# Kernel tuning notes

Hardware: AMD Instinct MI355X
Metric: run time of the kernel (lower is better)

Reference implementation:

```python
import jax, jax.numpy as jnp
import numpy as np

N = 100000   # nodes
E = 1600000  # edges
G = 2048     # graphs in batch
NF = 64      # node_feature_dim
D = 32       # hidden dim (hard-coded in module)
SF = 512     # solvent_feature_dim
BN_EPS = 1e-5


def setup_inputs() -> dict:
    key = jax.random.key(0)
    ks = jax.random.split(key, 24)
    s = 0.1
    return {
        "x": jax.random.normal(ks[0], (N, NF), jnp.float32),
        "edge_index": jax.random.randint(ks[1], (2, E), 0, N, dtype=jnp.int64),
        "batch": jnp.sort(jax.random.randint(ks[2], (N,), 0, G, dtype=jnp.int64)),
        "solvent_fingerprint": jax.random.uniform(ks[3], (G, SF), jnp.float32),
        # GIN layer 1 first Linear (NF->D); layers 2-5 first Linear stacked (D->D)
        "w1a": jax.random.normal(ks[4], (NF, D), jnp.float32) * s,
        "b1a": jnp.zeros((D,), jnp.float32),
        "ws_a": jax.random.normal(ks[5], (4, D, D), jnp.float32) * s,
        "bs_a": jnp.zeros((4, D), jnp.float32),
        # second Linear of all 5 GIN MLPs
        "ws_b": jax.random.normal(ks[6], (5, D, D), jnp.float32) * s,
        "bs_b": jnp.zeros((5, D), jnp.float32),
        # BatchNorm affine params per layer
        "bn_g": jnp.ones((5, D), jnp.float32),
        "bn_b": jnp.zeros((5, D), jnp.float32),
        # dense head
        "fcg_w": jax.random.normal(ks[7], (D, 128), jnp.float32) * s,
        "fcg_b": jnp.zeros((128,), jnp.float32),
        "fs1_w": jax.random.normal(ks[8], (SF, 256), jnp.float32) * s,
        "fs1_b": jnp.zeros((256,), jnp.float32),
        "fs2_w": jax.random.normal(ks[9], (256, 128), jnp.float32) * s,
        "fs2_b": jnp.zeros((128,), jnp.float32),
        "fc1_w": jax.random.normal(ks[10], (256, 1024), jnp.float32) * s,
        "fc1_b": jnp.zeros((1024,), jnp.float32),
        "fc2_w": jax.random.normal(ks[11], (1024, 256), jnp.float32) * s,
        "fc2_b": jnp.zeros((256,), jnp.float32),
        "out_w": jax.random.normal(ks[12], (256, 1), jnp.float32) * s,
        "out_b": jnp.zeros((1,), jnp.float32),
    }


def _bn_relu(h, g, b):
    # BatchNorm1d training-mode math (biased batch variance), then ReLU
    mu = h.mean(axis=0)
    var = h.var(axis=0)
    return jax.nn.relu((h - mu) * jax.lax.rsqrt(var + BN_EPS) * g + b)


def reference(x, edge_index, batch, solvent_fingerprint,
              w1a, b1a, ws_a, bs_a, ws_b, bs_b, bn_g, bn_b,
              fcg_w, fcg_b, fs1_w, fs1_b, fs2_w, fs2_b,
              fc1_w, fc1_b, fc2_w, fc2_b, out_w, out_b):
    src, dst = edge_index[0], edge_index[1]

    def gin_agg(h):
        # GINConv with eps=0: (1+eps)*x_i + sum_{j->i} x_j
        return h + jax.ops.segment_sum(h[src], dst, num_segments=N)

    # layer 1 (NF -> D)
    h = gin_agg(x)
    h = jax.nn.relu(h @ w1a + b1a) @ ws_b[0] + bs_b[0]
    h = _bn_relu(h, bn_g[0], bn_b[0])
    # layers 2-5 (D -> D)
    for i in range(4):
        h = gin_agg(h)
        h = jax.nn.relu(h @ ws_a[i] + bs_a[i]) @ ws_b[i + 1] + bs_b[i + 1]
        h = _bn_relu(h, bn_g[i + 1], bn_b[i + 1])

    pooled = jax.ops.segment_sum(h, batch, num_segments=G)  # [G, D]
    gfeat = jax.nn.relu(pooled @ fcg_w + fcg_b)             # dropout inactive (eval)

    sf = solvent_fingerprint.reshape(-1, SF)
    s = jax.nn.relu(sf @ fs1_w + fs1_b)
    s = jax.nn.relu(s @ fs2_w + fs2_b)

    z = jnp.concatenate([gfeat, s], axis=1)                 # [G, 256]
    z = jax.nn.relu(z @ fc1_w + fc1_b)
    z = jax.nn.relu(z @ fc2_w + fc2_b)
    return z @ out_w + out_b                                # [G, 1]
```

## Files before the change

kernel.cpp:

```cpp
#include <hip/hip_runtime.h>
#include <hip/hip_bf16.h>

static constexpr int N_NODES = 100000;
static constexpr int N_EDGES = 1600000;
static constexpr int N_GRAPH = 2048;
static constexpr float BN_EPS_C = 1e-5f;

static constexpr int BUCK_SHIFT = 9;
static constexpr int NB_BUCK = (N_NODES + 511) >> 9;
static constexpr int PART_B = 256;
static constexpr int CHUNK = N_EDGES / PART_B;
static constexpr int NTOT = NB_BUCK * PART_B;
static constexpr int NSLOT = 8;

typedef unsigned int uint;
typedef unsigned short ushort;


__device__ inline uint pk2(float a, float b) {
    uint ua = __float_as_uint(a), ub = __float_as_uint(b);
    ua = (ua + 0x7fffu + ((ua >> 16) & 1u)) >> 16;
    ub = (ub + 0x7fffu + ((ub >> 16) & 1u)) >> 16;
    return ua | (ub << 16);
}
__device__ inline float b2f_lo(uint u) { return __uint_as_float(u << 16); }
__device__ inline float b2f_hi(uint u) { return __uint_as_float(u & 0xffff0000u); }

__device__ inline void unpack8(uint4 v, float* f) {
    f[0] = b2f_lo(v.x); f[1] = b2f_hi(v.x);
    f[2] = b2f_lo(v.y); f[3] = b2f_hi(v.y);
    f[4] = b2f_lo(v.z); f[5] = b2f_hi(v.z);
    f[6] = b2f_lo(v.w); f[7] = b2f_hi(v.w);
}


__global__ __launch_bounds__(256) void k_bcount(const int* __restrict__ dst, int* __restrict__ cnt) {
    __shared__ int h[NB_BUCK];
    int blk = blockIdx.x, tid = threadIdx.x;
    for (int i = tid; i < NB_BUCK; i += 256) h[i] = 0;
    __syncthreads();
    int base = blk * CHUNK;
    for (int e = base + tid; e < base + CHUNK; e += 256) {
        int d = __builtin_nontemporal_load(&dst[e]);
        atomicAdd(&h[d >> BUCK_SHIFT], 1);
    }
    __syncthreads();
    for (int i = tid; i < NB_BUCK; i += 256) cnt[i * PART_B + blk] = h[i];
}

__global__ __launch_bounds__(256) void k_scan_partial2(const int* __restrict__ v, int* __restrict__ part, int n) {
    __shared__ int sw[4];
    int b = blockIdx.x, tid = threadIdx.x;
    int base = b * 1024;
    int s = 0;
#pragma unroll
    for (int r = 0; r < 4; ++r) {
        int i = base + r * 256 + tid;
        if (i < n) s += v[i];
    }
#pragma unroll
    for (int off = 32; off > 0; off >>= 1) s += __shfl_down(s, off);
    if ((tid & 63) == 0) sw[tid >> 6] = s;
    __syncthreads();
    if (tid == 0) part[b] = sw[0] + sw[1] + sw[2] + sw[3];
}

__global__ __launch_bounds__(256) void k_scan_offsets2(int* __restrict__ part, int nb, int* __restrict__ bstart) {
    __shared__ int sh[256];
    int tid = threadIdx.x;
    sh[tid] = (tid < nb) ? part[tid] : 0;
    __syncthreads();
    if (tid == 0) {
        int run = 0;
        for (int i = 0; i < nb; ++i) { int v = sh[i]; sh[i] = run; run += v; }
        bstart[NB_BUCK] = run;
    }
    __syncthreads();
    if (tid < nb) part[tid] = sh[tid];
}

__global__ __launch_bounds__(256) void k_scan_final2(int* __restrict__ cnt, const int* __restrict__ part,
                                                     int* __restrict__ bstart, int n) {
    __shared__ int wsum[4];
    int b = blockIdx.x, tid = threadIdx.x;
    int lane = tid & 63, w = tid >> 6;
    int base = b * 1024 + tid * 4;
    int v[4];
#pragma unroll
    for (int r = 0; r < 4; ++r) {
        int i = base + r;
        v[r] = (i < n) ? cnt[i] : 0;
    }
    int tsum = v[0] + v[1] + v[2] + v[3];
    int inc = tsum;
#pragma unroll
    for (int off = 1; off < 64; off <<= 1) {
        int t = __shfl_up(inc, off);
        if (lane >= off) inc += t;
    }
    if (lane == 63) wsum[w] = inc;
    __syncthreads();
    int woff = 0;
    for (int ww = 0; ww < w; ++ww) woff += wsum[ww];
    int run = part[b] + woff + (inc - tsum);
#pragma unroll
    for (int r = 0; r < 4; ++r) {
        int idx = base + r;
        if (idx < n) {
            int c = v[r];
            cnt[idx] = run;
            if ((idx & (PART_B - 1)) == 0) bstart[idx / PART_B] = run;
            run += c;
        }
    }
}

__global__ __launch_bounds__(256) void k_bpart(const int* __restrict__ src, const int* __restrict__ dst,
                                               const int* __restrict__ cnt, int2* __restrict__ ebuf) {
    __shared__ int cur[NB_BUCK];
    int blk = blockIdx.x, tid = threadIdx.x;
    for (int i = tid; i < NB_BUCK; i += 256) cur[i] = cnt[i * PART_B + blk];
    __syncthreads();
    int base = blk * CHUNK;
    for (int e = base + tid; e < base + CHUNK; e += 256) {
        int d = __builtin_nontemporal_load(&dst[e]);
        int s = __builtin_nontemporal_load(&src[e]);
        int p = atomicAdd(&cur[d >> BUCK_SHIFT], 1);
        ebuf[p] = make_int2(d, s);
    }
}

__global__ __launch_bounds__(256) void k_bfine(const int2* __restrict__ ebuf, const int* __restrict__ bstart,
                                               int* __restrict__ row_ptr, int* __restrict__ row_end,
                                               int* __restrict__ ssrc) {
    __shared__ int fh[512];
    __shared__ int wsum[4];
    int b = blockIdx.x, tid = threadIdx.x;
    int n0 = b << BUCK_SHIFT;
    int e0 = bstart[b], e1 = bstart[b + 1];
    fh[tid] = 0; fh[tid + 256] = 0;
    __syncthreads();
    for (int e = e0 + tid; e < e1; e += 256)
        atomicAdd(&fh[ebuf[e].x - n0], 1);
    __syncthreads();
    int a0 = fh[2 * tid], a1 = fh[2 * tid + 1];
    int s = a0 + a1;
    int lane = tid & 63, w = tid >> 6;
    int inc = s;
#pragma unroll
    for (int off = 1; off < 64; off <<= 1) {
        int t = __shfl_up(inc, off);
        if (lane >= off) inc += t;
    }
    if (lane == 63) wsum[w] = inc;
    __syncthreads();
    int woff = 0;
    for (int ww = 0; ww < w; ++ww) woff += wsum[ww];
    int excl = woff + inc - s;
    int p0 = excl, p1 = excl + a0;
    int node0 = n0 + 2 * tid, node1 = node0 + 1;
    if (node0 < N_NODES) { row_ptr[node0] = e0 + p0; row_end[node0] = e0 + p0 + a0; }
    if (node1 < N_NODES) { row_ptr[node1] = e0 + p1; row_end[node1] = e0 + p1 + a1; }
    fh[2 * tid] = p0; fh[2 * tid + 1] = p1;
    __syncthreads();
    for (int e = e0 + tid; e < e1; e += 256) {
        int2 v = ebuf[e];
        int p = atomicAdd(&fh[v.x - n0], 1);
        ssrc[e0 + p] = v.y;
    }
}


__global__ __launch_bounds__(256) void k_cvt_bf16(const float* __restrict__ x, ushort* __restrict__ xb, int n) {
    int i = (blockIdx.x * 256 + threadIdx.x) * 8;
    if (i >= n) return;
    float4 a = *(const float4*)(x + i);
    float4 b = *(const float4*)(x + i + 4);
    *(uint4*)(xb + i) = make_uint4(pk2(a.x, a.y), pk2(a.z, a.w), pk2(b.x, b.y), pk2(b.z, b.w));
}


__global__ __launch_bounds__(256) void k_fused1(const ushort* __restrict__ xb,
                                                const int* __restrict__ row_ptr, const int* __restrict__ row_end,
                                                const int* __restrict__ ssrc,
                                                const float* __restrict__ Wa, const float* __restrict__ ba,
                                                const float* __restrict__ Wb, const float* __restrict__ bb,
                                                ushort* __restrict__ uout, float* __restrict__ stats_out) {
    __shared__ float sWa[2048];
    __shared__ float sWb[1024];
    __shared__ float sba[32];
    __shared__ float sbb[32];
    __shared__ float bstats[64];
    int tid = threadIdx.x;
    for (int i = tid; i < 2048; i += 256) {
        int r = i >> 5, c = i & 31;
        sWa[(r << 5) + (c ^ (((r >> 3) & 7) << 2))] = Wa[i];
    }
    for (int i = tid; i < 1024; i += 256) sWb[i] = Wb[i];
    if (tid < 32) { sba[tid] = ba[tid]; sbb[tid] = bb[tid]; }
    if (tid < 64) bstats[tid] = 0.f;
    __syncthreads();

    int idx = blockIdx.x * 256 + tid;
    int node = idx >> 3;
    int sl = idx & 7;
    int f8 = sl * 8;
    bool active = node < N_NODES;

    float acc[8] = {0.f, 0.f, 0.f, 0.f, 0.f, 0.f, 0.f, 0.f};
    if (active) {
        unpack8(*(const uint4*)(xb + (size_t)node * 64 + f8), acc);
        int e = row_ptr[node], e1 = row_end[node];
        for (; e + 2 <= e1; e += 2) {
            int s0 = ssrc[e], s1 = ssrc[e + 1];
            uint4 va = *(const uint4*)(xb + (size_t)s0 * 64 + f8);
            uint4 vb = *(const uint4*)(xb + (size_t)s1 * 64 + f8);
            float v[8];
            unpack8(va, v);
#pragma unroll
            for (int j = 0; j < 8; ++j) acc[j] += v[j];
            unpack8(vb, v);
#pragma unroll
            for (int j = 0; j < 8; ++j) acc[j] += v[j];
        }
        if (e < e1) {
            int s = ssrc[e];
            float v[8];
            unpack8(*(const uint4*)(xb + (size_t)s * 64 + f8), v);
#pragma unroll
            for (int j = 0; j < 8; ++j) acc[j] += v[j];
        }
    }

    float pj[32];
#pragma unroll
    for (int j = 0; j < 32; ++j) pj[j] = 0.f;
    int sw = sl << 2;
#pragma unroll
    for (int kk = 0; kk < 8; ++kk) {
        float a = acc[kk];
        const float* rb = sWa + ((f8 + kk) << 5);
#pragma unroll
        for (int j4 = 0; j4 < 8; ++j4) {
            int jo = j4 << 2;
            float4 wv = *(const float4*)(rb + (jo ^ sw));
            pj[jo + 0] = fmaf(a, wv.x, pj[jo + 0]);
            pj[jo + 1] = fmaf(a, wv.y, pj[jo + 1]);
            pj[jo + 2] = fmaf(a, wv.z, pj[jo + 2]);
            pj[jo + 3] = fmaf(a, wv.w, pj[jo + 3]);
        }
    }
#pragma unroll
    for (int j = 0; j < 32; ++j) {
        pj[j] += __shfl_xor(pj[j], 1);
        pj[j] += __shfl_xor(pj[j], 2);
        pj[j] += __shfl_xor(pj[j], 4);
        pj[j] = fmaxf(pj[j] + sba[j], 0.f);
    }

    int j0 = sl * 4;
    float uu[4];
#pragma unroll
    for (int j = 0; j < 4; ++j) uu[j] = sbb[j0 + j];
#pragma unroll
    for (int k = 0; k < 32; ++k) {
        float a = pj[k];
        float4 wv = *(const float4*)(sWb + k * 32 + j0);
        uu[0] = fmaf(a, wv.x, uu[0]);
        uu[1] = fmaf(a, wv.y, uu[1]);
        uu[2] = fmaf(a, wv.z, uu[2]);
        uu[3] = fmaf(a, wv.w, uu[3]);
    }

    if (active) {
        uint2 pkv = make_uint2(pk2(uu[0], uu[1]), pk2(uu[2], uu[3]));
        *(uint2*)(uout + (size_t)node * 32 + j0) = pkv;
    } else {
#pragma unroll
        for (int j = 0; j < 4; ++j) uu[j] = 0.f;
    }

#pragma unroll
    for (int j = 0; j < 4; ++j) {
        float v = uu[j];
        float v2 = v * v;
        v += __shfl_xor(v, 8);  v2 += __shfl_xor(v2, 8);
        v += __shfl_xor(v, 16); v2 += __shfl_xor(v2, 16);
        v += __shfl_xor(v, 32); v2 += __shfl_xor(v2, 32);
        if ((tid & 63) < 8) {
            atomicAdd(&bstats[j0 + j], v);
            atomicAdd(&bstats[32 + j0 + j], v2);
        }
    }
    __syncthreads();
    if (tid < 64) atomicAdd(&stats_out[(blockIdx.x & (NSLOT - 1)) * 64 + tid], bstats[tid]);
}


__global__ __launch_bounds__(256) void k_fused(const ushort* __restrict__ uin, ushort* __restrict__ uout,
                                               const float* __restrict__ stats_in, float* __restrict__ stats_out,
                                               const float* __restrict__ bng, const float* __restrict__ bnb,
                                               const int* __restrict__ row_ptr, const int* __restrict__ row_end,
                                               const int* __restrict__ ssrc,
                                               const float* __restrict__ Wa, const float* __restrict__ ba,
                                               const float* __restrict__ Wb, const float* __restrict__ bb) {
    __shared__ float sWa[1024];
    __shared__ float sWb[1024];
    __shared__ float sba[32];
    __shared__ float sbb[32];
    __shared__ float bstats[64];
    int tid = threadIdx.x;
    for (int i = tid; i < 1024; i += 256) {
        int r = i >> 5, c = i & 31;
        sWa[(r << 5) + (c ^ (((r >> 3) & 3) << 2))] = Wa[i];
        sWb[i] = Wb[i];
    }
    if (tid < 32) { sba[tid] = ba[tid]; sbb[tid] = bb[tid]; }
    if (tid < 64) bstats[tid] = 0.f;
    __syncthreads();

    int idx = blockIdx.x * 256 + tid;
    int node = idx >> 2;
    int sl = idx & 3;
    int f8 = sl * 8;
    bool active = node < N_NODES;

    const float inv = 1.0f / (float)N_NODES;
    float sc[8], sh[8];
    {
        float s1[8] = {0,0,0,0,0,0,0,0}, s2[8] = {0,0,0,0,0,0,0,0};
        for (int s = 0; s < NSLOT; ++s) {
            const float* sp = stats_in + s * 64;
            float4 a = *(const float4*)(sp + f8);
            float4 b = *(const float4*)(sp + f8 + 4);
            float4 c = *(const float4*)(sp + 32 + f8);
            float4 d = *(const float4*)(sp + 36 + f8);
            s1[0] += a.x; s1[1] += a.y; s1[2] += a.z; s1[3] += a.w;
            s1[4] += b.x; s1[5] += b.y; s1[6] += b.z; s1[7] += b.w;
            s2[0] += c.x; s2[1] += c.y; s2[2] += c.z; s2[3] += c.w;
            s2[4] += d.x; s2[5] += d.y; s2[6] += d.z; s2[7] += d.w;
        }
        float g[8], b[8];
        *(float4*)g = *(const float4*)(bng + f8); *(float4*)(g + 4) = *(const float4*)(bng + f8 + 4);
        *(float4*)b = *(const float4*)(bnb + f8); *(float4*)(b + 4) = *(const float4*)(bnb + f8 + 4);
#pragma unroll
        for (int j = 0; j < 8; ++j) {
            float mu = s1[j] * inv;
            sc[j] = rsqrtf(s2[j] * inv - mu * mu + BN_EPS_C) * g[j];
            sh[j] = b[j] - mu * sc[j];
        }
    }

    float acc[8] = {0.f, 0.f, 0.f, 0.f, 0.f, 0.f, 0.f, 0.f};
    if (active) {
        float v[8];
        unpack8(*(const uint4*)(uin + (size_t)node * 32 + f8), v);
#pragma unroll
        for (int j = 0; j < 8; ++j) acc[j] = fmaxf(fmaf(v[j], sc[j], sh[j]), 0.f);
        int e = row_ptr[node], e1 = row_end[node];
        for (; e + 2 <= e1; e += 2) {
            int s0 = ssrc[e], s1 = ssrc[e + 1];
            uint4 va = *(const uint4*)(uin + (size_t)s0 * 32 + f8);
            uint4 vb = *(const uint4*)(uin + (size_t)s1 * 32 + f8);
            unpack8(va, v);
#pragma unroll
            for (int j = 0; j < 8; ++j) acc[j] += fmaxf(fmaf(v[j], sc[j], sh[j]), 0.f);
            unpack8(vb, v);
#pragma unroll
            for (int j = 0; j < 8; ++j) acc[j] += fmaxf(fmaf(v[j], sc[j], sh[j]), 0.f);
        }
        if (e < e1) {
            int s = ssrc[e];
            unpack8(*(const uint4*)(uin + (size_t)s * 32 + f8), v);
#pragma unroll
            for (int j = 0; j < 8; ++j) acc[j] += fmaxf(fmaf(v[j], sc[j], sh[j]), 0.f);
        }
    }

    float pj[32];
#pragma unroll
    for (int j = 0; j < 32; ++j) pj[j] = 0.f;
    int sw = sl << 2;
#pragma unroll
    for (int kk = 0; kk < 8; ++kk) {
        float a = acc[kk];
        const float* rb = sWa + ((f8 + kk) << 5);
#pragma unroll
        for (int j4 = 0; j4 < 8; ++j4) {
            int jo = j4 << 2;
            float4 wv = *(const float4*)(rb + (jo ^ sw));
            pj[jo + 0] = fmaf(a, wv.x, pj[jo + 0]);
            pj[jo + 1] = fmaf(a, wv.y, pj[jo + 1]);
            pj[jo + 2] = fmaf(a, wv.z, pj[jo + 2]);
            pj[jo + 3] = fmaf(a, wv.w, pj[jo + 3]);
        }
    }
#pragma unroll
    for (int j = 0; j < 32; ++j) {
        pj[j] += __shfl_xor(pj[j], 1);
        pj[j] += __shfl_xor(pj[j], 2);
        pj[j] = fmaxf(pj[j] + sba[j], 0.f);
    }

    float uu[8];
#pragma unroll
    for (int j = 0; j < 8; ++j) uu[j] = sbb[f8 + j];
#pragma unroll
    for (int k = 0; k < 32; ++k) {
        float a = pj[k];
        const float4* wr = (const float4*)(sWb + k * 32 + f8);
        float4 w0 = wr[0], w1 = wr[1];
        uu[0] = fmaf(a, w0.x, uu[0]);
        uu[1] = fmaf(a, w0.y, uu[1]);
        uu[2] = fmaf(a, w0.z, uu[2]);
        uu[3] = fmaf(a, w0.w, uu[3]);
        uu[4] = fmaf(a, w1.x, uu[4]);
        uu[5] = fmaf(a, w1.y, uu[5]);
        uu[6] = fmaf(a, w1.z, uu[6]);
        uu[7] = fmaf(a, w1.w, uu[7]);
    }

    if (active) {
        uint4 pkv = make_uint4(pk2(uu[0], uu[1]), pk2(uu[2], uu[3]), pk2(uu[4], uu[5]), pk2(uu[6], uu[7]));
        *(uint4*)(uout + (size_t)node * 32 + f8) = pkv;
    } else {
#pragma unroll
        for (int j = 0; j < 8; ++j) uu[j] = 0.f;
    }

#pragma unroll
    for (int j = 0; j < 8; ++j) {
        float v = uu[j];
        float v2 = v * v;
        v += __shfl_xor(v, 4);  v2 += __shfl_xor(v2, 4);
        v += __shfl_xor(v, 8);  v2 += __shfl_xor(v2, 8);
        v += __shfl_xor(v, 16); v2 += __shfl_xor(v2, 16);
        v += __shfl_xor(v, 32); v2 += __shfl_xor(v2, 32);
        if ((tid & 63) < 4) {
            atomicAdd(&bstats[f8 + j], v);
            atomicAdd(&bstats[32 + f8 + j], v2);
        }
    }
    __syncthreads();
    if (tid < 64) atomicAdd(&stats_out[(blockIdx.x & (NSLOT - 1)) * 64 + tid], bstats[tid]);
}


__global__ __launch_bounds__(256) void k_bn_pool(const ushort* __restrict__ u, const float* __restrict__ stats,
                                                 const float* __restrict__ bng, const float* __restrict__ bnb,
                                                 const int* __restrict__ batch, float* __restrict__ pooled) {
    const int CH = 128;
    int wid = (blockIdx.x * 256 + threadIdx.x) >> 6;
    int lane = threadIdx.x & 63;
    int f = lane & 31, par = lane >> 5;
    int n0 = wid * CH;
    if (n0 >= N_NODES) return;
    int n1 = n0 + CH; if (n1 > N_NODES) n1 = N_NODES;
    const float inv = 1.0f / (float)N_NODES;
    float sv = 0.f, sq = 0.f;
    for (int s = 0; s < NSLOT; ++s) { sv += stats[s * 64 + f]; sq += stats[s * 64 + 32 + f]; }
    float mu = sv * inv;
    float var = sq * inv - mu * mu;
    float sc = rsqrtf(var + BN_EPS_C) * bng[f];
    float sh = bnb[f] - mu * sc;
    float acc = 0.f;
    int curg = -1;
    for (int n = n0 + par; n < n1; n += 2) {
        int g = batch[n];
        if (g != curg) {
            if (curg >= 0) atomicAdd(&pooled[(size_t)curg * 32 + f], acc);
            acc = 0.f; curg = g;
        }
        float v = b2f_lo((uint)u[(size_t)n * 32 + f]);
        acc += fmaxf(fmaf(v, sc, sh), 0.f);
    }
    if (curg >= 0) atomicAdd(&pooled[(size_t)curg * 32 + f], acc);
}


#define GEMM_COMPUTE_16()                                                      \
    _Pragma("unroll")                                                          \
    for (int k = 0; k < 16; ++k) {                                             \
        float4 a4 = *(const float4*)&As[k][ty * 4];                            \
        float4 b4 = *(const float4*)&Bs[k][tx * 4];                            \
        acc[0][0] = fmaf(a4.x, b4.x, acc[0][0]);                               \
        acc[0][1] = fmaf(a4.x, b4.y, acc[0][1]);                               \
        acc[0][2] = fmaf(a4.x, b4.z, acc[0][2]);                               \
        acc[0][3] = fmaf(a4.x, b4.w, acc[0][3]);                               \
        acc[1][0] = fmaf(a4.y, b4.x, acc[1][0]);                               \
        acc[1][1] = fmaf(a4.y, b4.y, acc[1][1]);                               \
        acc[1][2] = fmaf(a4.y, b4.z, acc[1][2]);                               \
        acc[1][3] = fmaf(a4.y, b4.w, acc[1][3]);                               \
        acc[2][0] = fmaf(a4.z, b4.x, acc[2][0]);                               \
        acc[2][1] = fmaf(a4.z, b4.y, acc[2][1]);                               \
        acc[2][2] = fmaf(a4.z, b4.z, acc[2][2]);                               \
        acc[2][3] = fmaf(a4.z, b4.w, acc[2][3]);                               \
        acc[3][0] = fmaf(a4.w, b4.x, acc[3][0]);                               \
        acc[3][1] = fmaf(a4.w, b4.y, acc[3][1]);                               \
        acc[3][2] = fmaf(a4.w, b4.z, acc[3][2]);                               \
        acc[3][3] = fmaf(a4.w, b4.w, acc[3][3]);                               \
    }

__global__ __launch_bounds__(256) void k_gemm_f(const float* __restrict__ A, const float* __restrict__ B,
                                                const float* __restrict__ bias, float* __restrict__ C,
                                                int Nc, int K, int ldc, int do_relu) {
    __shared__ float As[16][64];
    __shared__ float Bs[16][64];
    int tid = threadIdx.x;
    int tx = tid & 15, ty = tid >> 4;
    int bm = blockIdx.x * 64, bn = blockIdx.y * 64;
    float acc[4][4] = {{0.f}};
    int am = tid >> 2;
    int ak = (tid & 3) * 4;
    int bk = tid >> 4;
    int bn4 = (tid & 15) * 4;
    const float* Ap = A + (size_t)(bm + am) * K + ak;
    const float* Bp = B + (size_t)bk * Nc + bn + bn4;
    float4 av = *(const float4*)Ap;
    float4 bv = *(const float4*)Bp;
    for (int k0 = 0; k0 < K; k0 += 16) {
        As[ak + 0][am] = av.x;
        As[ak + 1][am] = av.y;
        As[ak + 2][am] = av.z;
        As[ak + 3][am] = av.w;
        *(float4*)&Bs[bk][bn4] = bv;
        __syncthreads();
        if (k0 + 16 < K) {
            av = *(const float4*)(Ap + k0 + 16);
            bv = *(const float4*)(Bp + (size_t)(k0 + 16) * Nc);
        }
        GEMM_COMPUTE_16()
        __syncthreads();
    }
    float4 bi = *(const float4*)(bias + bn + tx * 4);
#pragma unroll
    for (int i = 0; i < 4; ++i) {
        float4 v;
        v.x = acc[i][0] + bi.x;
        v.y = acc[i][1] + bi.y;
        v.z = acc[i][2] + bi.z;
        v.w = acc[i][3] + bi.w;
        if (do_relu) {
            v.x = fmaxf(v.x, 0.f); v.y = fmaxf(v.y, 0.f);
            v.z = fmaxf(v.z, 0.f); v.w = fmaxf(v.w, 0.f);
        }
        *(float4*)(C + (size_t)(bm + ty * 4 + i) * ldc + bn + tx * 4) = v;
    }
}

__global__ __launch_bounds__(256) void k_gemm_p(const float* __restrict__ A, const float* __restrict__ B,
                                                float* __restrict__ psum, int Nc, int Ktot, int klen) {
    __shared__ float As[16][64];
    __shared__ float Bs[16][64];
    int tid = threadIdx.x;
    int tx = tid & 15, ty = tid >> 4;
    int bm = blockIdx.x * 64, bn = blockIdx.y * 64;
    int kb = blockIdx.z * klen;
    float acc[4][4] = {{0.f}};
    int am = tid >> 2;
    int ak = (tid & 3) * 4;
    int bk = tid >> 4;
    int bn4 = (tid & 15) * 4;
    const float* Ap = A + (size_t)(bm + am) * Ktot + kb + ak;
    const float* Bp = B + (size_t)(kb + bk) * Nc + bn + bn4;
    float4 av = *(const float4*)Ap;
    float4 bv = *(const float4*)Bp;
    for (int k0 = 0; k0 < klen; k0 += 16) {
        As[ak + 0][am] = av.x;
        As[ak + 1][am] = av.y;
        As[ak + 2][am] = av.z;
        As[ak + 3][am] = av.w;
        *(float4*)&Bs[bk][bn4] = bv;
        __syncthreads();
        if (k0 + 16 < klen) {
            av = *(const float4*)(Ap + k0 + 16);
            bv = *(const float4*)(Bp + (size_t)(k0 + 16) * Nc);
        }
        GEMM_COMPUTE_16()
        __syncthreads();
    }
    float* out = psum + (size_t)blockIdx.z * N_GRAPH * Nc;
#pragma unroll
    for (int i = 0; i < 4; ++i) {
        float4 v = make_float4(acc[i][0], acc[i][1], acc[i][2], acc[i][3]);
        *(float4*)(out + (size_t)(bm + ty * 4 + i) * Nc + bn + tx * 4) = v;
    }
}

__global__ __launch_bounds__(256) void k_reduce(const float* __restrict__ psum, const float* __restrict__ bias,
                                                float* __restrict__ C, int S, int Nc, int ldc, int do_relu) {
    int idx = blockIdx.x * 256 + threadIdx.x;
    int nq = Nc >> 2;
    if (idx >= N_GRAPH * nq) return;
    int m = idx / nq;
    int j = (idx - m * nq) * 4;
    float4 s = *(const float4*)(psum + (size_t)m * Nc + j);
    for (int z = 1; z < S; ++z) {
        float4 t = *(const float4*)(psum + (size_t)z * N_GRAPH * Nc + (size_t)m * Nc + j);
        s.x += t.x; s.y += t.y; s.z += t.z; s.w += t.w;
    }
    float4 bi = *(const float4*)(bias + j);
    s.x += bi.x; s.y += bi.y; s.z += bi.z; s.w += bi.w;
    if (do_relu) {
        s.x = fmaxf(s.x, 0.f); s.y = fmaxf(s.y, 0.f);
        s.z = fmaxf(s.z, 0.f); s.w = fmaxf(s.w, 0.f);
    }
    *(float4*)(C + (size_t)m * ldc + j) = s;
}


__global__ __launch_bounds__(256) void k_out(const float* __restrict__ z2, const float* __restrict__ w,
                                             const float* __restrict__ b, float* __restrict__ out) {
    int gid = blockIdx.x * 256 + threadIdx.x;
    int g = gid >> 6;
    int lane = threadIdx.x & 63;
    if (g >= N_GRAPH) return;
    float4 a = *(const float4*)(z2 + (size_t)g * 256 + lane * 4);
    float4 wv = *(const float4*)(w + lane * 4);
    float v = a.x * wv.x + a.y * wv.y + a.z * wv.z + a.w * wv.w;
#pragma unroll
    for (int off = 32; off > 0; off >>= 1) v += __shfl_down(v, off);
    if (lane == 0) out[g] = v + b[0];
}


extern "C" void kernel_launch(void* const* d_in, const int* in_sizes, int n_in,
                              void* d_out, int out_size, void* d_ws, size_t ws_size,
                              hipStream_t stream) {
    const float* x     = (const float*)d_in[0];
    const int*   eidx  = (const int*)d_in[1];
    const int*   batch = (const int*)d_in[2];
    const float* sf    = (const float*)d_in[3];
    const float* w1a   = (const float*)d_in[4];
    const float* b1a   = (const float*)d_in[5];
    const float* ws_a  = (const float*)d_in[6];
    const float* bs_a  = (const float*)d_in[7];
    const float* ws_b  = (const float*)d_in[8];
    const float* bs_b  = (const float*)d_in[9];
    const float* bn_g  = (const float*)d_in[10];
    const float* bn_b  = (const float*)d_in[11];
    const float* fcg_w = (const float*)d_in[12];
    const float* fcg_b = (const float*)d_in[13];
    const float* fs1_w = (const float*)d_in[14];
    const float* fs1_b = (const float*)d_in[15];
    const float* fs2_w = (const float*)d_in[16];
    const float* fs2_b = (const float*)d_in[17];
    const float* fc1_w = (const float*)d_in[18];
    const float* fc1_b = (const float*)d_in[19];
    const float* fc2_w = (const float*)d_in[20];
    const float* fc2_b = (const float*)d_in[21];
    const float* out_w = (const float*)d_in[22];
    const float* out_b = (const float*)d_in[23];
    float* dout = (float*)d_out;

    char* p = (char*)d_ws;
    float*  scr     = (float*)p;  p += (size_t)N_NODES * 64 * 4;
    ushort* u0      = (ushort*)p; p += (size_t)N_NODES * 32 * 2;
    ushort* u1      = (ushort*)p; p += (size_t)N_NODES * 32 * 2;
    int*    ssrc    = (int*)p;    p += (size_t)N_EDGES * 4;
    int*    row_ptr = (int*)p;    p += (size_t)N_NODES * 4;
    int*    row_end = (int*)p;    p += (size_t)N_NODES * 4;
    int*    cnt     = (int*)p;    p += (size_t)NTOT * 4;
    int*    part2   = (int*)p;    p += 512 * 4;
    int*    bstart  = (int*)p;    p += 256 * 4;
    float*  stats   = (float*)p;  p += (size_t)5 * NSLOT * 64 * 4;
    float*  pooled  = (float*)p;  p += (size_t)N_GRAPH * 32 * 4;
    ushort* xb      = (ushort*)p; p += (size_t)N_NODES * 64 * 2;

    int2* ebuf = (int2*)scr;

    float* zcat  = scr;
    float* z1buf = zcat + 2048 * 256;
    float* z2buf = z1buf + 2048 * 1024;
    float* s1buf = z2buf + 2048 * 256;
    float* psum  = s1buf + 2048 * 256;

    size_t zero_bytes = ((size_t)5 * NSLOT * 64 + (size_t)N_GRAPH * 32) * 4;
    hipMemsetAsync(stats, 0, zero_bytes, stream);

    const int* esrc = eidx;
    const int* edst = eidx + N_EDGES;

    const int scan_blocks = NTOT / 1024;
    k_bcount<<<PART_B, 256, 0, stream>>>(edst, cnt);
    k_scan_partial2<<<scan_blocks, 256, 0, stream>>>(cnt, part2, NTOT);
    k_scan_offsets2<<<1, 256, 0, stream>>>(part2, scan_blocks, bstart);
    k_scan_final2<<<scan_blocks, 256, 0, stream>>>(cnt, part2, bstart, NTOT);
    k_bpart<<<PART_B, 256, 0, stream>>>(esrc, edst, cnt, ebuf);
    k_bfine<<<NB_BUCK, 256, 0, stream>>>(ebuf, bstart, row_ptr, row_end, ssrc);

    const int SLOT_STRIDE = NSLOT * 64;

    k_cvt_bf16<<<(N_NODES * 64 / 8 + 255) / 256, 256, 0, stream>>>(x, xb, N_NODES * 64);
    k_fused1<<<(N_NODES * 8) / 256, 256, 0, stream>>>(xb, row_ptr, row_end, ssrc,
                                                      w1a, b1a, ws_b, bs_b, u0, stats);

    ushort* uin = u0;
    ushort* uout = u1;
    for (int L = 1; L <= 4; ++L) {
        k_fused<<<(N_NODES * 4 + 255) / 256, 256, 0, stream>>>(
            uin, uout,
            stats + (size_t)(L - 1) * SLOT_STRIDE, stats + (size_t)L * SLOT_STRIDE,
            bn_g + (L - 1) * 32, bn_b + (L - 1) * 32,
            row_ptr, row_end, ssrc,
            ws_a + (size_t)(L - 1) * 1024, bs_a + (L - 1) * 32,
            ws_b + (size_t)L * 1024, bs_b + L * 32);
        ushort* t = uin; uin = uout; uout = t;
    }

    {
        int waves = (N_NODES + 127) / 128;
        int blocks = (waves + 3) / 4;
        k_bn_pool<<<blocks, 256, 0, stream>>>(uin, stats + (size_t)4 * SLOT_STRIDE,
                                              bn_g + 128, bn_b + 128, batch, pooled);
    }

    k_gemm_f<<<dim3(32, 2), 256, 0, stream>>>(pooled, fcg_w, fcg_b, zcat, 128, 32, 256, 1);
    k_gemm_p<<<dim3(32, 4, 4), 256, 0, stream>>>(sf, fs1_w, psum, 256, 512, 128);
    k_reduce<<<512, 256, 0, stream>>>(psum, fs1_b, s1buf, 4, 256, 256, 1);
    k_gemm_p<<<dim3(32, 2, 4), 256, 0, stream>>>(s1buf, fs2_w, psum, 128, 256, 64);
    k_reduce<<<256, 256, 0, stream>>>(psum, fs2_b, zcat + 128, 4, 128, 256, 1);
    k_gemm_f<<<dim3(32, 16), 256, 0, stream>>>(zcat, fc1_w, fc1_b, z1buf, 1024, 256, 1024, 1);
    k_gemm_p<<<dim3(32, 4, 4), 256, 0, stream>>>(z1buf, fc2_w, psum, 256, 1024, 256);
    k_reduce<<<512, 256, 0, stream>>>(psum, fc2_b, z2buf, 4, 256, 256, 1);
    k_out<<<512, 256, 0, stream>>>(z2buf, out_w, out_b, dout);
}
```

Before: 566.9 us.

## Project layer-1 features to 32 dims before aggregation, unroll gathers by four

Uses linearity of the GIN sum to apply the first 64->32 Linear to x before neighbour aggregation (k_xw1), so the layer-1 gather reads 32-dim bf16 rows instead of 64-dim ones. This halves gather traffic over 1.6M edges and drops the separate bf16 conversion kernel, at the cost of an extra kernel and a second matmul restructured through a shared-memory tile. The edge loops in both the layer-1 and later-layer kernels are also unrolled by four to put more loads in flight. Rounding order changes slightly because the projection is rounded to bf16 before summation.

```diff
diff --git a/kernel.cpp b/kernel.cpp
--- a/kernel.cpp
+++ b/kernel.cpp
@@ -171,65 +171,31 @@
 }
 
 
-__global__ __launch_bounds__(256) void k_cvt_bf16(const float* __restrict__ x, ushort* __restrict__ xb, int n) {
-    int i = (blockIdx.x * 256 + threadIdx.x) * 8;
-    if (i >= n) return;
-    float4 a = *(const float4*)(x + i);
-    float4 b = *(const float4*)(x + i + 4);
-    *(uint4*)(xb + i) = make_uint4(pk2(a.x, a.y), pk2(a.z, a.w), pk2(b.x, b.y), pk2(b.z, b.w));
-}
-
-
-__global__ __launch_bounds__(256) void k_fused1(const ushort* __restrict__ xb,
-                                                const int* __restrict__ row_ptr, const int* __restrict__ row_end,
-                                                const int* __restrict__ ssrc,
-                                                const float* __restrict__ Wa, const float* __restrict__ ba,
-                                                const float* __restrict__ Wb, const float* __restrict__ bb,
-                                                ushort* __restrict__ uout, float* __restrict__ stats_out) {
+__global__ __launch_bounds__(256) void k_xw1(const float* __restrict__ x, const float* __restrict__ Wa,
+                                             ushort* __restrict__ y) {
     __shared__ float sWa[2048];
-    __shared__ float sWb[1024];
-    __shared__ float sba[32];
-    __shared__ float sbb[32];
-    __shared__ float bstats[64];
     int tid = threadIdx.x;
     for (int i = tid; i < 2048; i += 256) {
         int r = i >> 5, c = i & 31;
-        sWa[(r << 5) + (c ^ (((r >> 3) & 7) << 2))] = Wa[i];
-    }
-    for (int i = tid; i < 1024; i += 256) sWb[i] = Wb[i];
-    if (tid < 32) { sba[tid] = ba[tid]; sbb[tid] = bb[tid]; }
-    if (tid < 64) bstats[tid] = 0.f;
-    __syncthreads();
-
+        sWa[(r << 5) + (c ^ (((r >> 4) & 3) << 2))] = Wa[i];
+    }
+    __syncthreads();
     int idx = blockIdx.x * 256 + tid;
-    int node = idx >> 3;
-    int sl = idx & 7;
-    int f8 = sl * 8;
+    int node = idx >> 2;
+    int sl = idx & 3;
+    int k0 = sl * 16;
     bool active = node < N_NODES;
 
-    float acc[8] = {0.f, 0.f, 0.f, 0.f, 0.f, 0.f, 0.f, 0.f};
+    float xv[16];
     if (active) {
-        unpack8(*(const uint4*)(xb + (size_t)node * 64 + f8), acc);
-        int e = row_ptr[node], e1 = row_end[node];
-        for (; e + 2 <= e1; e += 2) {
-            int s0 = ssrc[e], s1 = ssrc[e + 1];
-            uint4 va = *(const uint4*)(xb + (size_t)s0 * 64 + f8);
-            uint4 vb = *(const uint4*)(xb + (size_t)s1 * 64 + f8);
-            float v[8];
-            unpack8(va, v);
-#pragma unroll
-            for (int j = 0; j < 8; ++j) acc[j] += v[j];
-            unpack8(vb, v);
-#pragma unroll
-            for (int j = 0; j < 8; ++j) acc[j] += v[j];
-        }
-        if (e < e1) {
-            int s = ssrc[e];
-            float v[8];
-            unpack8(*(const uint4*)(xb + (size_t)s * 64 + f8), v);
-#pragma unroll
-            for (int j = 0; j < 8; ++j) acc[j] += v[j];
-        }
+        const float* xr = x + (size_t)node * 64 + k0;
+        *(float4*)(xv + 0)  = *(const float4*)(xr + 0);
+        *(float4*)(xv + 4)  = *(const float4*)(xr + 4);
+        *(float4*)(xv + 8)  = *(const float4*)(xr + 8);
+        *(float4*)(xv + 12) = *(const float4*)(xr + 12);
+    } else {
+#pragma unroll
+        for (int j = 0; j < 16; ++j) xv[j] = 0.f;
     }
 
     float pj[32];
@@ -237,9 +203,9 @@
     for (int j = 0; j < 32; ++j) pj[j] = 0.f;
     int sw = sl << 2;
 #pragma unroll
-    for (int kk = 0; kk < 8; ++kk) {
-        float a = acc[kk];
-        const float* rb = sWa + ((f8 + kk) << 5);
+    for (int kk = 0; kk < 16; ++kk) {
+        float a = xv[kk];
+        const float* rb = sWa + ((k0 + kk) << 5);
 #pragma unroll
         for (int j4 = 0; j4 < 8; ++j4) {
             int jo = j4 << 2;
@@ -254,42 +220,126 @@
     for (int j = 0; j < 32; ++j) {
         pj[j] += __shfl_xor(pj[j], 1);
         pj[j] += __shfl_xor(pj[j], 2);
-        pj[j] += __shfl_xor(pj[j], 4);
-        pj[j] = fmaxf(pj[j] + sba[j], 0.f);
-    }
-
-    int j0 = sl * 4;
-    float uu[4];
-#pragma unroll
-    for (int j = 0; j < 4; ++j) uu[j] = sbb[j0 + j];
-#pragma unroll
-    for (int k = 0; k < 32; ++k) {
-        float a = pj[k];
-        float4 wv = *(const float4*)(sWb + k * 32 + j0);
-        uu[0] = fmaf(a, wv.x, uu[0]);
-        uu[1] = fmaf(a, wv.y, uu[1]);
-        uu[2] = fmaf(a, wv.z, uu[2]);
-        uu[3] = fmaf(a, wv.w, uu[3]);
-    }
-
+    }
+    if (active && sl == 0) {
+        uint pk[16];
+#pragma unroll
+        for (int j = 0; j < 16; ++j) pk[j] = pk2(pj[2 * j], pj[2 * j + 1]);
+        uint4* yp = (uint4*)(y + (size_t)node * 32);
+        yp[0] = make_uint4(pk[0], pk[1], pk[2], pk[3]);
+        yp[1] = make_uint4(pk[4], pk[5], pk[6], pk[7]);
+        yp[2] = make_uint4(pk[8], pk[9], pk[10], pk[11]);
+        yp[3] = make_uint4(pk[12], pk[13], pk[14], pk[15]);
+    }
+}
+
+
+__global__ __launch_bounds__(256) void k_fused1y(const ushort* __restrict__ y,
+                                                 const int* __restrict__ row_ptr, const int* __restrict__ row_end,
+                                                 const int* __restrict__ ssrc,
+                                                 const float* __restrict__ ba,
+                                                 const float* __restrict__ Wb, const float* __restrict__ bb,
+                                                 ushort* __restrict__ uout, float* __restrict__ stats_out) {
+    __shared__ float sWb[1024];
+    __shared__ float sba[32];
+    __shared__ float sbb[32];
+    __shared__ float bstats[64];
+    __shared__ float tile[64][36];
+    int tid = threadIdx.x;
+    for (int i = tid; i < 1024; i += 256) sWb[i] = Wb[i];
+    if (tid < 32) { sba[tid] = ba[tid]; sbb[tid] = bb[tid]; }
+    if (tid < 64) bstats[tid] = 0.f;
+    __syncthreads();
+
+    int idx = blockIdx.x * 256 + tid;
+    int node = idx >> 2;
+    int sl = idx & 3;
+    int f8 = sl * 8;
+    int nloc = tid >> 2;
+    bool active = node < N_NODES;
+
+    float acc[8] = {0.f, 0.f, 0.f, 0.f, 0.f, 0.f, 0.f, 0.f};
     if (active) {
-        uint2 pkv = make_uint2(pk2(uu[0], uu[1]), pk2(uu[2], uu[3]));
-        *(uint2*)(uout + (size_t)node * 32 + j0) = pkv;
+        unpack8(*(const uint4*)(y + (size_t)node * 32 + f8), acc);
+        int e = row_ptr[node], e1 = row_end[node];
+        float v[8];
+        for (; e + 4 <= e1; e += 4) {
+            int s0 = ssrc[e], s1 = ssrc[e + 1], s2 = ssrc[e + 2], s3 = ssrc[e + 3];
+            uint4 va = *(const uint4*)(y + (size_t)s0 * 32 + f8);
+            uint4 vb = *(const uint4*)(y + (size_t)s1 * 32 + f8);
+            uint4 vc = *(const uint4*)(y + (size_t)s2 * 32 + f8);
+            uint4 vd = *(const uint4*)(y + (size_t)s3 * 32 + f8);
+            unpack8(va, v);
+#pragma unroll
+            for (int j = 0; j < 8; ++j) acc[j] += v[j];
+            unpack8(vb, v);
+#pragma unroll
+            for (int j = 0; j < 8; ++j) acc[j] += v[j];
+            unpack8(vc, v);
+#pragma unroll
+            for (int j = 0; j < 8; ++j) acc[j] += v[j];
+            unpack8(vd, v);
+#pragma unroll
+            for (int j = 0; j < 8; ++j) acc[j] += v[j];
+        }
+        for (; e < e1; ++e) {
+            int s = ssrc[e];
+            unpack8(*(const uint4*)(y + (size_t)s * 32 + f8), v);
+#pragma unroll
+            for (int j = 0; j < 8; ++j) acc[j] += v[j];
+        }
+    }
+
+    float h8[8];
+#pragma unroll
+    for (int j = 0; j < 8; ++j) h8[j] = fmaxf(acc[j] + sba[f8 + j], 0.f);
+    *(float4*)&tile[nloc][f8] = make_float4(h8[0], h8[1], h8[2], h8[3]);
+    *(float4*)&tile[nloc][f8 + 4] = make_float4(h8[4], h8[5], h8[6], h8[7]);
+    __syncthreads();
+
+    float uu[8];
+#pragma unroll
+    for (int j = 0; j < 8; ++j) uu[j] = sbb[f8 + j];
+#pragma unroll
+    for (int k4 = 0; k4 < 8; ++k4) {
+        float4 hv = *(const float4*)&tile[nloc][k4 * 4];
+        float hvv[4] = {hv.x, hv.y, hv.z, hv.w};
+#pragma unroll
+        for (int m = 0; m < 4; ++m) {
+            int k = k4 * 4 + m;
+            float a = hvv[m];
+            const float4* wr = (const float4*)(sWb + k * 32 + f8);
+            float4 w0 = wr[0], w1 = wr[1];
+            uu[0] = fmaf(a, w0.x, uu[0]);
+            uu[1] = fmaf(a, w0.y, uu[1]);
+            uu[2] = fmaf(a, w0.z, uu[2]);
+            uu[3] = fmaf(a, w0.w, uu[3]);
+            uu[4] = fmaf(a, w1.x, uu[4]);
+            uu[5] = fmaf(a, w1.y, uu[5]);
+            uu[6] = fmaf(a, w1.z, uu[6]);
+            uu[7] = fmaf(a, w1.w, uu[7]);
+        }
+    }
+
+    if (active) {
+        uint4 pkv = make_uint4(pk2(uu[0], uu[1]), pk2(uu[2], uu[3]), pk2(uu[4], uu[5]), pk2(uu[6], uu[7]));
+        *(uint4*)(uout + (size_t)node * 32 + f8) = pkv;
     } else {
 #pragma unroll
-        for (int j = 0; j < 4; ++j) uu[j] = 0.f;
-    }
-
-#pragma unroll
-    for (int j = 0; j < 4; ++j) {
+        for (int j = 0; j < 8; ++j) uu[j] = 0.f;
+    }
+
+#pragma unroll
+    for (int j = 0; j < 8; ++j) {
         float v = uu[j];
         float v2 = v * v;
+        v += __shfl_xor(v, 4);  v2 += __shfl_xor(v2, 4);
         v += __shfl_xor(v, 8);  v2 += __shfl_xor(v2, 8);
         v += __shfl_xor(v, 16); v2 += __shfl_xor(v2, 16);
         v += __shfl_xor(v, 32); v2 += __shfl_xor(v2, 32);
-        if ((tid & 63) < 8) {
-            atomicAdd(&bstats[j0 + j], v);
-            atomicAdd(&bstats[32 + j0 + j], v2);
+        if ((tid & 63) < 4) {
+            atomicAdd(&bstats[f8 + j], v);
+            atomicAdd(&bstats[32 + f8 + j], v2);
         }
     }
     __syncthreads();
@@ -358,18 +408,26 @@
 #pragma unroll
         for (int j = 0; j < 8; ++j) acc[j] = fmaxf(fmaf(v[j], sc[j], sh[j]), 0.f);
         int e = row_ptr[node], e1 = row_end[node];
-        for (; e + 2 <= e1; e += 2) {
-            int s0 = ssrc[e], s1 = ssrc[e + 1];
+        for (; e + 4 <= e1; e += 4) {
+            int s0 = ssrc[e], s1 = ssrc[e + 1], s2 = ssrc[e + 2], s3 = ssrc[e + 3];
             uint4 va = *(const uint4*)(uin + (size_t)s0 * 32 + f8);
             uint4 vb = *(const uint4*)(uin + (size_t)s1 * 32 + f8);
+            uint4 vc = *(const uint4*)(uin + (size_t)s2 * 32 + f8);
+            uint4 vd = *(const uint4*)(uin + (size_t)s3 * 32 + f8);
             unpack8(va, v);
 #pragma unroll
             for (int j = 0; j < 8; ++j) acc[j] += fmaxf(fmaf(v[j], sc[j], sh[j]), 0.f);
             unpack8(vb, v);
 #pragma unroll
             for (int j = 0; j < 8; ++j) acc[j] += fmaxf(fmaf(v[j], sc[j], sh[j]), 0.f);
-        }
-        if (e < e1) {
+            unpack8(vc, v);
+#pragma unroll
+            for (int j = 0; j < 8; ++j) acc[j] += fmaxf(fmaf(v[j], sc[j], sh[j]), 0.f);
+            unpack8(vd, v);
+#pragma unroll
+            for (int j = 0; j < 8; ++j) acc[j] += fmaxf(fmaf(v[j], sc[j], sh[j]), 0.f);
+        }
+        for (; e < e1; ++e) {
             int s = ssrc[e];
             unpack8(*(const uint4*)(uin + (size_t)s * 32 + f8), v);
 #pragma unroll
@@ -665,7 +723,7 @@
     int*    bstart  = (int*)p;    p += 256 * 4;
     float*  stats   = (float*)p;  p += (size_t)5 * NSLOT * 64 * 4;
     float*  pooled  = (float*)p;  p += (size_t)N_GRAPH * 32 * 4;
-    ushort* xb      = (ushort*)p; p += (size_t)N_NODES * 64 * 2;
+    ushort* ybuf    = (ushort*)p; p += (size_t)N_NODES * 32 * 2;
 
     int2* ebuf = (int2*)scr;
 
@@ -690,15 +748,16 @@
     k_bfine<<<NB_BUCK, 256, 0, stream>>>(ebuf, bstart, row_ptr, row_end, ssrc);
 
     const int SLOT_STRIDE = NSLOT * 64;
-
-    k_cvt_bf16<<<(N_NODES * 64 / 8 + 255) / 256, 256, 0, stream>>>(x, xb, N_NODES * 64);
-    k_fused1<<<(N_NODES * 8) / 256, 256, 0, stream>>>(xb, row_ptr, row_end, ssrc,
-                                                      w1a, b1a, ws_b, bs_b, u0, stats);
+    const int nblk4 = (N_NODES * 4 + 255) / 256;
+
+    k_xw1<<<nblk4, 256, 0, stream>>>(x, w1a, ybuf);
+    k_fused1y<<<nblk4, 256, 0, stream>>>(ybuf, row_ptr, row_end, ssrc,
+                                         b1a, ws_b, bs_b, u0, stats);
 
     ushort* uin = u0;
     ushort* uout = u1;
     for (int L = 1; L <= 4; ++L) {
-        k_fused<<<(N_NODES * 4 + 255) / 256, 256, 0, stream>>>(
+        k_fused<<<nblk4, 256, 0, stream>>>(
             uin, uout,
             stats + (size_t)(L - 1) * SLOT_STRIDE, stats + (size_t)L * SLOT_STRIDE,
             bn_g + (L - 1) * 32, bn_b + (L - 1) * 32,
```

Result: faster. 525.0 us (-7.4%).
